# Optimization experiments

Measured on AMD Instinct MI355X. Metric: run time of the kernel, lower is better.

## Reference

```python
import jax, jax.numpy as jnp
import numpy as np
from jax import lax

H_IMG, W_IMG = 1280, 1280
STRIDES = (8, 16, 32, 64, 128)
FEAT_SHAPES = tuple((H_IMG // s) * (W_IMG // s) for s in STRIDES)  # (25600,6400,1600,400,100)
N_POINTS = sum(FEAT_SHAPES)  # 34100
NUM_CLASSES = 1
TOPK = 1000
SCORE_THRESH = 0.05
NMS_THRESH = 0.5
MAX_DET = 300
BATCH = 8
N_GT = 200


def make_points():
    # matches AnchorFreePS.reference_points: cell centers at stride*i + stride//2, (cx, cy) order
    pts = []
    for s in STRIDES:
        h, w = H_IMG // s, W_IMG // s
        cx = np.arange(w, dtype=np.float32) * s + s // 2
        cy = np.arange(h, dtype=np.float32) * s + s // 2
        gy, gx = np.meshgrid(cy, cx, indexing='ij')
        pts.append(np.stack([gx, gy], axis=-1).reshape(-1, 2))
    return jnp.asarray(np.concatenate(pts, axis=0))


def setup_inputs() -> dict:
    key = jax.random.key(0)
    k1, k2, k3, k4 = jax.random.split(key, 4)
    points = make_points()  # [N,2]
    xy = jax.random.uniform(k1, (BATCH, N_GT, 2), minval=0.0, maxval=1000.0)
    wh = jax.random.uniform(k2, (BATCH, N_GT, 2), minval=20.0, maxval=260.0)
    gt_boxes = jnp.concatenate([xy, xy + wh], axis=-1)  # [B,M,4] x1y1x2y2
    cls_logits = jax.random.normal(k3, (BATCH, N_POINTS, NUM_CLASSES)) * 1.5 - 3.0
    regression = jax.random.uniform(k4, (BATCH, N_POINTS, 4)) * 0.1  # normalized ltrb codes
    return {"points": points, "gt_boxes": gt_boxes, "cls_logits": cls_logits, "regression": regression}


def match_points_to_boxes(points, gt_boxes):
    # point-in-box test + area-cost argmin (compute_loss matched_idxs)
    px = points[None, :, None, 0]  # [1,N,1]
    py = points[None, :, None, 1]
    b = gt_boxes[:, None, :, :]    # [B,1,M,4]
    inside = (px >= b[..., 0]) & (px <= b[..., 2]) & (py >= b[..., 1]) & (py <= b[..., 3])  # [B,N,M]
    matched = jnp.any(inside, axis=-1)  # [B,N]
    areas = (gt_boxes[..., 2] - gt_boxes[..., 0]) * (gt_boxes[..., 3] - gt_boxes[..., 1])  # [B,M]
    BIG = jnp.float32(2 ** 31 - 1)  # torch.iinfo(torch.int).max
    cost = jnp.where(inside, areas[:, None, :], BIG)
    idx = jnp.argmin(cost, axis=-1)
    return jnp.where(matched, idx, -1)


def decode_boxes(rel, pts):
    # FCOSBoxCoder.decode_single with weights (1,1,1,1)
    l = rel[:, 0] * W_IMG
    t = rel[:, 1] * H_IMG
    r = rel[:, 2] * W_IMG
    b = rel[:, 3] * H_IMG
    x, y = pts[:, 0], pts[:, 1]
    return jnp.stack([x - l, y - t, x + r, y + b], axis=-1)


def clip_boxes(boxes):
    return jnp.stack([
        jnp.clip(boxes[:, 0], 0.0, W_IMG),
        jnp.clip(boxes[:, 1], 0.0, H_IMG),
        jnp.clip(boxes[:, 2], 0.0, W_IMG),
        jnp.clip(boxes[:, 3], 0.0, H_IMG)], axis=-1)


def nms(boxes, scores, labels, valid_init):
    # fixed-size sequential NMS equivalent to batched_nms (same-label suppression)
    work = lax.stop_gradient(jnp.where(valid_init, scores, -jnp.inf))

    def body(w, _):
        i = jnp.argmax(w)
        s = w[i]
        box = boxes[i]
        x1 = jnp.maximum(box[0], boxes[:, 0])
        y1 = jnp.maximum(box[1], boxes[:, 1])
        x2 = jnp.minimum(box[2], boxes[:, 2])
        y2 = jnp.minimum(box[3], boxes[:, 3])
        inter = jnp.clip(x2 - x1, 0.0) * jnp.clip(y2 - y1, 0.0)
        a1 = (box[2] - box[0]) * (box[3] - box[1])
        a2 = (boxes[:, 2] - boxes[:, 0]) * (boxes[:, 3] - boxes[:, 1])
        iou = inter / (a1 + a2 - inter + 1e-9)
        supp = (iou > NMS_THRESH) & (labels == labels[i])
        w = jnp.where(supp, -jnp.inf, w).at[i].set(-jnp.inf)
        return w, (i, s)

    _, (idxs, picked) = lax.scan(body, work, None, length=MAX_DET)
    valid = picked > -jnp.inf
    return idxs, valid


def postprocess_image(points, cls_i, reg_i):
    bx_list, sc_list, lb_list = [], [], []
    off = 0
    for size in FEAT_SHAPES:  # fixed small level loop
        sl = slice(off, off + size)
        off += size
        scores = jax.nn.sigmoid(cls_i[sl]).reshape(-1)  # [size*C]
        k = min(TOPK, size * NUM_CLASSES)
        sc, idx = lax.top_k(scores, k)
        a = idx // NUM_CLASSES
        lb = idx % NUM_CLASSES
        bx = clip_boxes(decode_boxes(reg_i[sl][a], points[sl][a]))
        bx_list.append(bx)
        sc_list.append(sc)
        lb_list.append(lb)
    boxes = jnp.concatenate(bx_list, axis=0)
    scores = jnp.concatenate(sc_list, axis=0)
    labels = jnp.concatenate(lb_list, axis=0)
    idxs, valid = nms(boxes, scores, labels, scores > SCORE_THRESH)
    out_boxes = jnp.where(valid[:, None], boxes[idxs], 0.0)
    out_scores = jnp.where(valid, scores[idxs], 0.0)
    out_labels = jnp.where(valid, labels[idxs], -1)
    return out_boxes, out_scores, out_labels, valid


def reference(points, gt_boxes, cls_logits, regression):
    matched_idxs = match_points_to_boxes(points, gt_boxes)  # [B,N]
    boxes, scores, labels, valid = jax.vmap(
        lambda c, r: postprocess_image(points, c, r))(cls_logits, regression)
    return matched_idxs, boxes, scores, labels, valid
```

## Files before the change

kernel.cpp:

```cpp
#include <hip/hip_runtime.h>
#include <stdint.h>

#define N_POINTS   34100
#define BATCH      8
#define N_GT       200
#define NLEV       5
#define NCAND      3500
#define MAX_DET    300
#define SCORE_TH   0.05f
#define NMS_TH     0.5f
#define IMG        1280.0f
#define NBIN       4096
#define TIE_CAP    4096
#define MTH 0.50000002980232238769531250

#define OUT_MATCH  0
#define OUT_BOXES  272800
#define OUT_SCORES 282400
#define OUT_LABELS 284800
#define OUT_VALID  287200

#define WS_SBOX    2632192
#define WS_SSC     3080192
#define WS_MASK    3192192
#define WS_DIAG    9500032
#define MASK_STRIDE 98560
#define DIAG_STRIDE 3520

typedef unsigned long long u64;
typedef uint32_t u32;

__device__ __forceinline__ int mask_off(int c) {
    int g = c >> 6;
    return 64 * (55 * g - (g * (g - 1)) / 2) + (c - (g << 6)) * (55 - g);
}

__device__ __forceinline__ int level_of(int p) {
    return (p < 25600) ? 0 : (p < 32000) ? 1 : (p < 33600) ? 2 : (p < 34000) ? 3 : 4;
}
__device__ __forceinline__ int loff_of(int l) {
    return (l == 0) ? 0 : (l == 1) ? 25600 : (l == 2) ? 32000 : (l == 3) ? 33600 : 34000;
}
__device__ __forceinline__ int k_of(int l) {
    return (l == 0) ? 1000 : (l == 1) ? 1000 : (l == 2) ? 1000 : (l == 3) ? 400 : 100;
}
__device__ __forceinline__ u64 readlane64(u64 v, int t) {
    u32 lo = (u32)__builtin_amdgcn_readlane((int)(u32)v, t);
    u32 hi = (u32)__builtin_amdgcn_readlane((int)(u32)(v >> 32), t);
    return ((u64)hi << 32) | lo;
}
__device__ __forceinline__ u32 sigkey(float lg) {
    float s = 1.0f / (1.0f + expf(-lg));
    u32 u = __float_as_uint(s);
    return (u & 0x80000000u) ? ~u : (u | 0x80000000u);
}

#define MPT 2
__global__ __launch_bounds__(256)
void match_kernel(const float* __restrict__ points,
                  const float* __restrict__ gt,
                  float* __restrict__ out_match) {
#pragma clang fp contract(off)
    __shared__ float bx1[N_GT], by1[N_GT], bx2[N_GT], by2[N_GT], ar[N_GT];
    const int b = blockIdx.y;
    const int base = blockIdx.x * (256 * MPT) + threadIdx.x;

    for (int j = threadIdx.x; j < N_GT; j += 256) {
        float x1 = gt[(b * N_GT + j) * 4 + 0];
        float y1 = gt[(b * N_GT + j) * 4 + 1];
        float x2 = gt[(b * N_GT + j) * 4 + 2];
        float y2 = gt[(b * N_GT + j) * 4 + 3];
        bx1[j] = x1; by1[j] = y1; bx2[j] = x2; by2[j] = y2;
        ar[j] = (x2 - x1) * (y2 - y1);
    }
    __syncthreads();

    const float BIGF = 2147483648.0f;
    float px[MPT], py[MPT], best[MPT];
    int bi[MPT];
#pragma unroll
    for (int k = 0; k < MPT; ++k) {
        int p = base + k * 256;
        int pc = (p < N_POINTS) ? p : 0;
        px[k] = points[pc * 2 + 0];
        py[k] = points[pc * 2 + 1];
        best[k] = BIGF; bi[k] = -1;
    }
    for (int j = 0; j < N_GT; ++j) {
        float x1 = bx1[j], y1 = by1[j], x2 = bx2[j], y2 = by2[j], a = ar[j];
#pragma unroll
        for (int k = 0; k < MPT; ++k) {
            bool inside = (px[k] >= x1) && (px[k] <= x2) &&
                          (py[k] >= y1) && (py[k] <= y2);
            float cost = inside ? a : BIGF;
            if (cost < best[k]) { best[k] = cost; bi[k] = j; }
        }
    }
#pragma unroll
    for (int k = 0; k < MPT; ++k) {
        int p = base + k * 256;
        if (p < N_POINTS) out_match[b * N_POINTS + p] = (float)bi[k];
    }
}

#define SORT_T 1024
__global__ __launch_bounds__(SORT_T)
void pipeline_kernel(const float* __restrict__ logits,
                     const float* __restrict__ reg,
                     const float* __restrict__ points,
                     float* __restrict__ sboxes,
                     float* __restrict__ sscores) {
#pragma clang fp contract(off)
    __shared__ __align__(16) char smem[131072];
    u64* sk   = (u64*)smem;
    u32* hist = (u32*)(smem + 32768);
    u64* tb   = (u64*)(smem + 32768);
    u64* aux  = (u64*)(smem + 65536);
    u32* h    = (u32*)(smem + 98304);
    u32* bs   = (u32*)(smem + 114688);
    __shared__ u32 sTl[NLEV], skkl[NLEV], wt[16];
    __shared__ u32 scnt, stcnt;

    const int b = blockIdx.x;
    const int tid = threadIdx.x;
    const int lane = tid & 63;
    const int wid = tid >> 6;
    const float* lg = logits + b * N_POINTS;

    for (int i = tid; i < NLEV * NBIN; i += SORT_T) hist[i] = 0u;
    if (tid == 0) { scnt = 0u; stcnt = 0u; }
    __syncthreads();
    for (int i = tid; i < N_POINTS; i += SORT_T) {
        u32 key = sigkey(lg[i]);
        atomicAdd(&hist[level_of(i) * NBIN + ((key >> 19) & 4095u)], 1u);
    }
    __syncthreads();

    if (wid < NLEV) {
        const u32 K = (u32)k_of(wid);
        const u32* hh = hist + wid * NBIN;
        u32 S = 0;
#pragma unroll 8
        for (int i = 0; i < 64; ++i) S += hh[lane * 64 + i];
        u32 acc = S;
#pragma unroll
        for (int off = 1; off < 64; off <<= 1) {
            u32 v = (u32)__shfl_down((int)acc, off);
            if (lane + off < 64) acc += v;
        }
        u32 sfxAfter = acc - S;
        bool hit = (sfxAfter < K) && (sfxAfter + S >= K);
        u64 bal = __ballot(hit);
        int Lg = (int)__builtin_ctzll(bal);
        u32 sfxG = (u32)__shfl((int)sfxAfter, Lg);

        u32 v = hh[Lg * 64 + lane];
        u32 acc2 = v;
#pragma unroll
        for (int off = 1; off < 64; off <<= 1) {
            u32 t = (u32)__shfl_down((int)acc2, off);
            if (lane + off < 64) acc2 += t;
        }
        u32 sfx2 = sfxG + acc2 - v;
        bool hit2 = (sfx2 < K) && (sfx2 + v >= K);
        if (hit2) { sTl[wid] = (u32)(Lg * 64 + lane); skkl[wid] = K - sfx2; }
    }
    __syncthreads();

    const u64 below = (lane == 0) ? 0ull : (~0ull >> (64 - lane));
    for (int i0 = tid; i0 - tid < N_POINTS; i0 += SORT_T) {
        bool active = i0 < N_POINTS;
        int pc = active ? i0 : (N_POINTS - 1);
        u32 key = sigkey(lg[pc]);
        int l = level_of(pc);
        u32 digit = (key >> 19) & 4095u;
        u32 T = sTl[l];
        bool isDef = active && (digit > T);
        bool isTie = active && (digit == T);
        u64 k50 = ((u64)key << 18) | ((u64)(7 - l) << 15)
                | (u64)(32767 - (pc - loff_of(l)));
        u64 grp = __ballot(isDef);
        if (grp) {
            int leader = (int)__builtin_ctzll(grp);
            u32 base_ = 0;
            if (lane == leader)
                base_ = atomicAdd(&scnt, (u32)__builtin_popcountll(grp));
            base_ = (u32)__shfl((int)base_, leader);
            if (isDef) sk[base_ + (u32)__builtin_popcountll(grp & below)] = k50;
        }
        u64 tg = __ballot(isTie);
        if (tg) {
            int leader = (int)__builtin_ctzll(tg);
            u32 base_ = 0;
            if (lane == leader)
                base_ = atomicAdd(&stcnt, (u32)__builtin_popcountll(tg));
            base_ = (u32)__shfl((int)base_, leader);
            if (isTie) {
                u32 pos = base_ + (u32)__builtin_popcountll(tg & below);
                if (pos < TIE_CAP) tb[pos] = k50;
            }
        }
    }
    __syncthreads();

    int t = (int)stcnt; if (t > TIE_CAP) t = TIE_CAP;
    for (int j0 = tid; j0 - tid < t; j0 += SORT_T) {
        bool active = j0 < t;
        u64 kj = active ? tb[j0] : 0ull;
        u32 lvtag = (u32)(kj >> 15) & 7u;
        int r = 0;
        for (int i = 0; i < t; ++i) {
            u64 ki = tb[i];
            r += (ki > kj && (((u32)(ki >> 15) & 7u) == lvtag)) ? 1 : 0;
        }
        bool inc = active && (r < (int)skkl[7 - lvtag]);
        u64 grp = __ballot(inc);
        if (grp) {
            int leader = (int)__builtin_ctzll(grp);
            u32 base_ = 0;
            if (lane == leader)
                base_ = atomicAdd(&scnt, (u32)__builtin_popcountll(grp));
            base_ = (u32)__shfl((int)base_, leader);
            if (inc) sk[base_ + (u32)__builtin_popcountll(grp & below)] = kj;
        }
    }
    __syncthreads();
    const int total = (int)scnt;

    for (int i = tid; i < NBIN; i += SORT_T) h[i] = 0u;
    __syncthreads();
    for (int i = tid; i < total; i += SORT_T)
        atomicAdd(&h[(u32)(sk[i] >> 37) & 4095u], 1u);
    __syncthreads();

    u32 t0 = h[4095 - 4 * tid];
    u32 t1 = h[4095 - (4 * tid + 1)];
    u32 t2 = h[4095 - (4 * tid + 2)];
    u32 t3 = h[4095 - (4 * tid + 3)];
    u32 tsum = t0 + t1 + t2 + t3;
    u32 sc_ = tsum;
#pragma unroll
    for (int off = 1; off < 64; off <<= 1) {
        u32 v = (u32)__shfl_up((int)sc_, off);
        if (lane >= off) sc_ += v;
    }
    if (lane == 63) wt[wid] = sc_;
    __syncthreads();
    if (tid < 64) {
        u32 v = (tid < 16) ? wt[tid] : 0u;
        u32 s2 = v;
#pragma unroll
        for (int off = 1; off < 16; off <<= 1) {
            u32 x = (u32)__shfl_up((int)s2, off);
            if (tid >= off) s2 += x;
        }
        if (tid < 16) wt[tid] = s2 - v;
    }
    __syncthreads();
    u32 run = (sc_ - tsum) + wt[wid];
    bs[4095 - 4 * tid] = run;       run += t0;
    bs[4095 - (4 * tid + 1)] = run; run += t1;
    bs[4095 - (4 * tid + 2)] = run; run += t2;
    bs[4095 - (4 * tid + 3)] = run;
    __syncthreads();
    for (int i = tid; i < NBIN; i += SORT_T) h[i] = 0u;
    __syncthreads();
    for (int i = tid; i < total; i += SORT_T) {
        u64 k = sk[i];
        u32 d = (u32)(k >> 37) & 4095u;
        u32 pos = bs[d] + atomicAdd(&h[d], 1u);
        aux[pos] = k;
    }
    __syncthreads();
    for (int p = tid; p < total; p += SORT_T) {
        u64 kp = aux[p];
        u32 d = (u32)(kp >> 37) & 4095u;
        u32 gbase = bs[d];
        u32 gend = (d == 0) ? (u32)total : bs[d - 1];
        u32 r = 0;
        for (u32 q = gbase; q < gend; ++q) r += (aux[q] > kp) ? 1u : 0u;
        sk[gbase + r] = kp;
    }
    __syncthreads();

    for (int r = tid; r < NCAND; r += SORT_T) {
        float x1 = 0.f, y1 = 0.f, x2 = 0.f, y2 = 0.f, sc = 0.f;
        if (r < total) {
            u64 k50 = sk[r];
            int lowb = (int)(k50 & 0x3FFFFull);
            int l = 7 - (lowb >> 15);
            int idxl = 32767 - (lowb & 32767);
            int p = loff_of(l) + idxl;
            u32 key32 = (u32)(k50 >> 18);
            sc = __uint_as_float(key32 ^ 0x80000000u);
            int gp = b * N_POINTS + p;
            float l_ = reg[gp * 4 + 0] * IMG;
            float t_ = reg[gp * 4 + 1] * IMG;
            float r_ = reg[gp * 4 + 2] * IMG;
            float bb = reg[gp * 4 + 3] * IMG;
            float px = points[p * 2 + 0];
            float py = points[p * 2 + 1];
            x1 = fminf(fmaxf(px - l_, 0.0f), IMG);
            y1 = fminf(fmaxf(py - t_, 0.0f), IMG);
            x2 = fminf(fmaxf(px + r_, 0.0f), IMG);
            y2 = fminf(fmaxf(py + bb, 0.0f), IMG);
        }
        int slot = b * NCAND + r;
        sboxes[slot * 4 + 0] = x1;
        sboxes[slot * 4 + 1] = y1;
        sboxes[slot * 4 + 2] = x2;
        sboxes[slot * 4 + 3] = y2;
        sscores[slot] = sc;
    }
}

__global__ __launch_bounds__(256)
void mask_kernel(const float* __restrict__ sboxes,
                 const float* __restrict__ sscores,
                 u64* __restrict__ mask,
                 u64* __restrict__ diag) {
#pragma clang fp contract(off)
    const int b = blockIdx.y;
    const int wv = threadIdx.x >> 6;
    const int lane = threadIdx.x & 63;
    const int NG = (NCAND + 3) >> 2;
    const int gidx = blockIdx.x * 4 + wv;
    if (gidx >= NG) return;
    const int c0 = gidx << 2;

    const float4* gb = (const float4*)sboxes + b * NCAND;
    const float* gs = sscores + b * NCAND;
    u64* mout = mask + (size_t)b * MASK_STRIDE;
    u64* dout = diag + (size_t)b * DIAG_STRIDE;

    float4 bc[4]; float a1[4]; bool ok[4]; int g[4]; u64* rp[4];
    bool any = false;
#pragma unroll
    for (int i = 0; i < 4; ++i) {
        int c = c0 + i;
        int cc = (c < NCAND) ? c : (NCAND - 1);
        bc[i] = gb[cc];
        a1[i] = (bc[i].z - bc[i].x) * (bc[i].w - bc[i].y);
        ok[i] = (c < NCAND) && (gs[cc] > SCORE_TH);
        g[i] = cc >> 6;
        rp[i] = mout + mask_off(cc) - g[i];
        any |= ok[i];
    }
    if (!any) return;

    for (int w = (c0 >> 6); w < 55; ++w) {
        int cj = (w << 6) + lane;
        float4 bj = (cj < NCAND) ? gb[cj] : make_float4(0.f, 0.f, 0.f, 0.f);
        float a2 = (bj.z - bj.x) * (bj.w - bj.y);
#pragma unroll
        for (int i = 0; i < 4; ++i) {
            float x1 = fmaxf(bc[i].x, bj.x);
            float y1 = fmaxf(bc[i].y, bj.y);
            float x2 = fminf(bc[i].z, bj.z);
            float y2 = fminf(bc[i].w, bj.w);
            float inter = fmaxf(x2 - x1, 0.f) * fmaxf(y2 - y1, 0.f);
            float denom = a1[i] + a2 - inter + 1e-9f;
            float hf = 0.5f * denom;
            float rr = fmaf(0x1p-25f, denom, hf);
            u64 bits = __ballot(inter > rr);
            u64 eq = __ballot(inter == rr);
            if (eq) {
                u64 fb = __ballot((double)inter > MTH * (double)denom);
                bits |= (eq & fb);
            }
            if (lane == 0 && ok[i] && w >= g[i]) {
                rp[i][w] = bits;
                if (w == g[i]) dout[c0 + i] = bits;
            }
        }
    }
}

__global__ __launch_bounds__(64)
void scan_kernel(const float* __restrict__ sboxes,
                 const float* __restrict__ sscores,
                 const u64* __restrict__ mask,
                 const u64* __restrict__ diag,
                 float* __restrict__ out) {
    const int b = blockIdx.x;
    const int lane = threadIdx.x;
    const float4* gb = (const float4*)sboxes + b * NCAND;
    const float* gs = sscores + b * NCAND;
    const u64* mrow = mask + (size_t)b * MASK_STRIDE;
    const u64* drow = diag + (size_t)b * DIAG_STRIDE;

    float* ob = out + OUT_BOXES  + b * MAX_DET * 4;
    float* os = out + OUT_SCORES + b * MAX_DET;
    float* ol = out + OUT_LABELS + b * MAX_DET;
    float* ov = out + OUT_VALID  + b * MAX_DET;

    u64 m = 0ull;
    u64 rowN = drow[lane];
    float4 bjN = gb[lane];
    float sjN = gs[lane];

    int kept = 0;
    for (int w = 0; w < 55; ++w) {
        const int wbase = w << 6;
        const u64 row = rowN;
        const float4 bj = bjN;
        const float sj = sjN;
        if (w < 54) {
            int cn = wbase + 64 + lane;
            int cc = (cn < NCAND) ? cn : (NCAND - 1);
            rowN = drow[cc];
            bjN = gb[cc];
            float s = gs[cc];
            sjN = (cn < NCAND) ? s : 0.f;
        }
        int c = wbase + lane;
        u64 bad = __ballot(!((c < NCAND) && (sj > SCORE_TH)));
        u64 cur = readlane64(m, w) | bad;
        u64 km = 0ull;
        while (kept < MAX_DET) {
            u64 avail = ~cur;
            if (avail == 0ull) break;
            int t = (int)__builtin_ctzll(avail);
            u64 r = readlane64(row, t);
            cur |= r | (1ull << t);
            km |= 1ull << t;
            if (lane == t) {
                ob[kept * 4 + 0] = bj.x;
                ob[kept * 4 + 1] = bj.y;
                ob[kept * 4 + 2] = bj.z;
                ob[kept * 4 + 3] = bj.w;
                os[kept] = sj;
                ol[kept] = 0.0f;
                ov[kept] = 1.0f;
            }
            kept++;
        }
        if (km) {
            const bool lr = (lane >= w && lane < 55);
            const int lo = lane - w;
            u64 acc = 0ull;
            while (km) {
#define POPBIT(tn) int tn = -1; if (km) { tn = (int)__builtin_ctzll(km); km &= km - 1ull; }
                POPBIT(t0) POPBIT(t1) POPBIT(t2) POPBIT(t3)
                POPBIT(t4) POPBIT(t5) POPBIT(t6) POPBIT(t7)
#undef POPBIT
                u64 v0 = 0, v1 = 0, v2 = 0, v3 = 0, v4 = 0, v5 = 0, v6 = 0, v7 = 0;
                if (lr) {
                    v0 = mrow[mask_off(wbase + t0) + lo];
                    if (t1 >= 0) v1 = mrow[mask_off(wbase + t1) + lo];
                    if (t2 >= 0) v2 = mrow[mask_off(wbase + t2) + lo];
                    if (t3 >= 0) v3 = mrow[mask_off(wbase + t3) + lo];
                    if (t4 >= 0) v4 = mrow[mask_off(wbase + t4) + lo];
                    if (t5 >= 0) v5 = mrow[mask_off(wbase + t5) + lo];
                    if (t6 >= 0) v6 = mrow[mask_off(wbase + t6) + lo];
                    if (t7 >= 0) v7 = mrow[mask_off(wbase + t7) + lo];
                }
                acc |= ((v0 | v1) | (v2 | v3)) | ((v4 | v5) | (v6 | v7));
            }
            m |= acc;
        }
        if (kept >= MAX_DET) break;
    }
    for (int k = kept + lane; k < MAX_DET; k += 64) {
        ob[k * 4 + 0] = 0.f; ob[k * 4 + 1] = 0.f;
        ob[k * 4 + 2] = 0.f; ob[k * 4 + 3] = 0.f;
        os[k] = 0.f; ol[k] = -1.f; ov[k] = 0.f;
    }
}

extern "C" void kernel_launch(void* const* d_in, const int* in_sizes, int n_in,
                              void* d_out, int out_size, void* d_ws, size_t ws_size,
                              hipStream_t stream) {
    const float* points = (const float*)d_in[0];
    const float* gt     = (const float*)d_in[1];
    const float* logits = (const float*)d_in[2];
    const float* reg    = (const float*)d_in[3];
    float* out = (float*)d_out;

    float* sboxes  = (float*)((char*)d_ws + WS_SBOX);
    float* sscores = (float*)((char*)d_ws + WS_SSC);
    u64* mask   = (u64*)((char*)d_ws + WS_MASK);
    u64* diag   = (u64*)((char*)d_ws + WS_DIAG);

    pipeline_kernel<<<BATCH, SORT_T, 0, stream>>>(logits, reg, points,
                                                  sboxes, sscores);

    dim3 g1((N_POINTS + 256 * MPT - 1) / (256 * MPT), BATCH);
    match_kernel<<<g1, 256, 0, stream>>>(points, gt, out + OUT_MATCH);

    dim3 g5(((NCAND + 3) / 4 + 3) / 4, BATCH);
    mask_kernel<<<g5, 256, 0, stream>>>(sboxes, sscores, mask, diag);

    scan_kernel<<<BATCH, 64, 0, stream>>>(sboxes, sscores, mask, diag, out);
}
```

Measured before the change: 279.9 us.

## Precompute sigmoid keys in match kernel and balance mask triangle work

```diff
diff --git a/kernel.cpp b/kernel.cpp
--- a/kernel.cpp
+++ b/kernel.cpp
@@ -20,6 +20,7 @@
 #define OUT_LABELS 284800
 #define OUT_VALID  287200
 
+#define WS_KEYS    0
 #define WS_SBOX    2632192
 #define WS_SSC     3080192
 #define WS_MASK    3192192
@@ -49,17 +50,14 @@
     u32 hi = (u32)__builtin_amdgcn_readlane((int)(u32)(v >> 32), t);
     return ((u64)hi << 32) | lo;
 }
-__device__ __forceinline__ u32 sigkey(float lg) {
-    float s = 1.0f / (1.0f + expf(-lg));
-    u32 u = __float_as_uint(s);
-    return (u & 0x80000000u) ? ~u : (u | 0x80000000u);
-}
 
 #define MPT 2
 __global__ __launch_bounds__(256)
-void match_kernel(const float* __restrict__ points,
-                  const float* __restrict__ gt,
-                  float* __restrict__ out_match) {
+void match_key_kernel(const float* __restrict__ points,
+                      const float* __restrict__ gt,
+                      const float* __restrict__ logits,
+                      float* __restrict__ out_match,
+                      u32* __restrict__ keys) {
 #pragma clang fp contract(off)
     __shared__ float bx1[N_GT], by1[N_GT], bx2[N_GT], by2[N_GT], ar[N_GT];
     const int b = blockIdx.y;
@@ -99,13 +97,19 @@
 #pragma unroll
     for (int k = 0; k < MPT; ++k) {
         int p = base + k * 256;
-        if (p < N_POINTS) out_match[b * N_POINTS + p] = (float)bi[k];
+        if (p >= N_POINTS) continue;
+        out_match[b * N_POINTS + p] = (float)bi[k];
+        float lg = logits[b * N_POINTS + p];
+        float s = 1.0f / (1.0f + expf(-lg));
+        u32 u = __float_as_uint(s);
+        u32 key = (u & 0x80000000u) ? ~u : (u | 0x80000000u);
+        keys[b * N_POINTS + p] = key;
     }
 }
 
 #define SORT_T 1024
 __global__ __launch_bounds__(SORT_T)
-void pipeline_kernel(const float* __restrict__ logits,
+void pipeline_kernel(const u32* __restrict__ keys,
                      const float* __restrict__ reg,
                      const float* __restrict__ points,
                      float* __restrict__ sboxes,
@@ -125,13 +129,13 @@
     const int tid = threadIdx.x;
     const int lane = tid & 63;
     const int wid = tid >> 6;
-    const float* lg = logits + b * N_POINTS;
+    const u32* kk_ = keys + b * N_POINTS;
 
     for (int i = tid; i < NLEV * NBIN; i += SORT_T) hist[i] = 0u;
     if (tid == 0) { scnt = 0u; stcnt = 0u; }
     __syncthreads();
     for (int i = tid; i < N_POINTS; i += SORT_T) {
-        u32 key = sigkey(lg[i]);
+        u32 key = kk_[i];
         atomicAdd(&hist[level_of(i) * NBIN + ((key >> 19) & 4095u)], 1u);
     }
     __syncthreads();
@@ -171,7 +175,7 @@
     for (int i0 = tid; i0 - tid < N_POINTS; i0 += SORT_T) {
         bool active = i0 < N_POINTS;
         int pc = active ? i0 : (N_POINTS - 1);
-        u32 key = sigkey(lg[pc]);
+        u32 key = kk_[pc];
         int l = level_of(pc);
         u32 digit = (key >> 19) & 4095u;
         u32 T = sTl[l];
@@ -324,53 +328,59 @@
     const int wv = threadIdx.x >> 6;
     const int lane = threadIdx.x & 63;
     const int NG = (NCAND + 3) >> 2;
+    const int NH = (NG + 1) >> 1;
     const int gidx = blockIdx.x * 4 + wv;
-    if (gidx >= NG) return;
-    const int c0 = gidx << 2;
+    if (gidx >= NH) return;
 
     const float4* gb = (const float4*)sboxes + b * NCAND;
     const float* gs = sscores + b * NCAND;
     u64* mout = mask + (size_t)b * MASK_STRIDE;
     u64* dout = diag + (size_t)b * DIAG_STRIDE;
 
-    float4 bc[4]; float a1[4]; bool ok[4]; int g[4]; u64* rp[4];
-    bool any = false;
-#pragma unroll
-    for (int i = 0; i < 4; ++i) {
-        int c = c0 + i;
-        int cc = (c < NCAND) ? c : (NCAND - 1);
-        bc[i] = gb[cc];
-        a1[i] = (bc[i].z - bc[i].x) * (bc[i].w - bc[i].y);
-        ok[i] = (c < NCAND) && (gs[cc] > SCORE_TH);
-        g[i] = cc >> 6;
-        rp[i] = mout + mask_off(cc) - g[i];
-        any |= ok[i];
-    }
-    if (!any) return;
-
-    for (int w = (c0 >> 6); w < 55; ++w) {
-        int cj = (w << 6) + lane;
-        float4 bj = (cj < NCAND) ? gb[cj] : make_float4(0.f, 0.f, 0.f, 0.f);
-        float a2 = (bj.z - bj.x) * (bj.w - bj.y);
+    for (int s = 0; s < 2; ++s) {
+        const int g0 = (s == 0) ? gidx : (NG - 1 - gidx);
+        if (s == 1 && g0 == gidx) break;
+        const int c0 = g0 << 2;
+
+        float4 bc[4]; float a1[4]; bool ok[4]; int g[4]; u64* rp[4];
+        bool any = false;
 #pragma unroll
         for (int i = 0; i < 4; ++i) {
-            float x1 = fmaxf(bc[i].x, bj.x);
-            float y1 = fmaxf(bc[i].y, bj.y);
-            float x2 = fminf(bc[i].z, bj.z);
-            float y2 = fminf(bc[i].w, bj.w);
-            float inter = fmaxf(x2 - x1, 0.f) * fmaxf(y2 - y1, 0.f);
-            float denom = a1[i] + a2 - inter + 1e-9f;
-            float hf = 0.5f * denom;
-            float rr = fmaf(0x1p-25f, denom, hf);
-            u64 bits = __ballot(inter > rr);
-            u64 eq = __ballot(inter == rr);
-            if (eq) {
-                u64 fb = __ballot((double)inter > MTH * (double)denom);
-                bits |= (eq & fb);
-            }
-            if (lane == 0 && ok[i] && w >= g[i]) {
-                rp[i][w] = bits;
-                if (w == g[i]) dout[c0 + i] = bits;
+            int c = c0 + i;
+            int cc = (c < NCAND) ? c : (NCAND - 1);
+            bc[i] = gb[cc];
+            a1[i] = (bc[i].z - bc[i].x) * (bc[i].w - bc[i].y);
+            ok[i] = (c < NCAND) && (gs[cc] > SCORE_TH);
+            g[i] = cc >> 6;
+            rp[i] = mout + mask_off(cc) - g[i];
+            any |= ok[i];
+        }
+        if (!any) continue;
+
+        for (int w = (c0 >> 6); w < 55; ++w) {
+            int cj = (w << 6) + lane;
+            float4 bj = (cj < NCAND) ? gb[cj] : make_float4(0.f, 0.f, 0.f, 0.f);
+            float a2 = (bj.z - bj.x) * (bj.w - bj.y);
+#pragma unroll
+            for (int i = 0; i < 4; ++i) {
+                float x1 = fmaxf(bc[i].x, bj.x);
+                float y1 = fmaxf(bc[i].y, bj.y);
+                float x2 = fminf(bc[i].z, bj.z);
+                float y2 = fminf(bc[i].w, bj.w);
+                float inter = fmaxf(x2 - x1, 0.f) * fmaxf(y2 - y1, 0.f);
+                float denom = a1[i] + a2 - inter + 1e-9f;
+                float hf = 0.5f * denom;
+                float rr = fmaf(0x1p-25f, denom, hf);
+                u64 bits = __ballot(inter > rr);
+                u64 eq = __ballot(inter == rr);
+                if (eq) {
+                    u64 fb = __ballot((double)inter > MTH * (double)denom);
+                    bits |= (eq & fb);
+                }
+                if (lane == 0 && ok[i] && w >= g[i]) {
+                    rp[i][w] = bits;
+                    if (w == g[i]) dout[c0 + i] = bits;
+                }
             }
         }
     }
@@ -477,18 +487,20 @@
     const float* reg    = (const float*)d_in[3];
     float* out = (float*)d_out;
 
+    u32* keys      = (u32*)((char*)d_ws + WS_KEYS);
     float* sboxes  = (float*)((char*)d_ws + WS_SBOX);
     float* sscores = (float*)((char*)d_ws + WS_SSC);
     u64* mask   = (u64*)((char*)d_ws + WS_MASK);
     u64* diag   = (u64*)((char*)d_ws + WS_DIAG);
 
-    pipeline_kernel<<<BATCH, SORT_T, 0, stream>>>(logits, reg, points,
+    dim3 g1((N_POINTS + 256 * MPT - 1) / (256 * MPT), BATCH);
+    match_key_kernel<<<g1, 256, 0, stream>>>(points, gt, logits,
+                                             out + OUT_MATCH, keys);
+
+    pipeline_kernel<<<BATCH, SORT_T, 0, stream>>>(keys, reg, points,
                                                   sboxes, sscores);
 
-    dim3 g1((N_POINTS + 256 * MPT - 1) / (256 * MPT), BATCH);
-    match_kernel<<<g1, 256, 0, stream>>>(points, gt, out + OUT_MATCH);
-
-    dim3 g5(((NCAND + 3) / 4 + 3) / 4, BATCH);
+    dim3 g5((((NCAND + 3) / 4 + 1) / 2 + 3) / 4, BATCH);
     mask_kernel<<<g5, 256, 0, stream>>>(sboxes, sscores, mask, diag);
 
     scan_kernel<<<BATCH, 64, 0, stream>>>(sboxes, sscores, mask, diag, out);
```

After: 263.9 us. 5.7% less time.
